# Performance work log

Measured on AMD Instinct MI355X. Metric: run time of the kernel, lower is better.

## Reference

```python
import jax, jax.numpy as jnp
import numpy as np

# Polynomial coefficients (len(thetas)=4 polys, k=3 -> 2 propagation hops each); K=1
THETAS = [[0.5, -0.4, 0.1], [0.25, 0.5, -0.25], [0.1, 0.3, 0.6], [0.05, -0.2, 0.8]]
K = 1
N_NODES = 100000
N_EDGES = 1600000
IN_FEATS = 32
OUT_FEATS = 64


def setup_inputs() -> dict:
    key = jax.random.key(0)
    ks = jax.random.split(key, 10)
    feat = jax.random.normal(ks[0], (N_NODES, IN_FEATS), dtype=jnp.float32)
    edge_src = jax.random.randint(ks[1], (N_EDGES,), 0, N_NODES)
    edge_dst = jax.random.randint(ks[2], (N_EDGES,), 0, N_NODES)
    labels = jax.random.randint(ks[3], (N_NODES,), 0, 2)
    s = 0.05
    W_lin = jax.random.normal(ks[4], (IN_FEATS * len(THETAS), OUT_FEATS), dtype=jnp.float32) * s
    b_lin = jax.random.normal(ks[5], (OUT_FEATS,), dtype=jnp.float32) * s
    W_lin1 = jax.random.normal(ks[6], (IN_FEATS * len(THETAS), OUT_FEATS), dtype=jnp.float32) * s
    b_lin1 = jax.random.normal(ks[7], (OUT_FEATS,), dtype=jnp.float32) * s
    W_transh = jax.random.normal(ks[8], (IN_FEATS, OUT_FEATS), dtype=jnp.float32) * s
    b_transh = jax.random.normal(ks[9], (OUT_FEATS,), dtype=jnp.float32) * s
    return {"feat": feat, "edge_src": edge_src, "edge_dst": edge_dst, "labels": labels,
            "W_lin": W_lin, "b_lin": b_lin, "W_lin1": W_lin1, "b_lin1": b_lin1,
            "W_transh": W_transh, "b_transh": b_transh}


def _poly_group(thetas, feat0, D_invsqrt, edge_src, edge_dst, mask, n_nodes):
    """Signed polynomial Laplacian propagation.
    Each hop: feat <- feat - scatter_sum_dst(mask * (feat*Dinv)[src]) * Dinv.
    feat carries over across thetas within a group (as in the original loop).
    """
    def prop(f):
        h = f * D_invsqrt                       # [N, F]
        m = h[edge_src]                         # gather [E, F]
        if mask is not None:
            m = m * mask[:, None]
        agg = jax.ops.segment_sum(m, edge_dst, num_segments=n_nodes)
        return f - agg * D_invsqrt

    hs = []
    f = feat0
    for th in thetas:
        h = th[0] * f
        for k in range(1, len(th)):
            f = prop(f)
            h = h + th[k] * f
        hs.append(h)
    return hs


def reference(feat, edge_src, edge_dst, labels, W_lin, b_lin, W_lin1, b_lin1, W_transh, b_transh):
    n_nodes = feat.shape[0]
    # edge sign from label agreement
    pos_mask = (labels[edge_src] == labels[edge_dst]).astype(feat.dtype)  # [E]
    neg_mask = 1.0 - pos_mask
    seg = lambda v: jax.ops.segment_sum(v, edge_dst, num_segments=n_nodes)
    deg = seg(jnp.ones_like(pos_mask))
    pos_deg = seg(pos_mask)
    neg_deg = seg(neg_mask)
    dinv = lambda d: jnp.power(jnp.clip(d, 1.0, None), -0.5)[:, None]
    D_o, D_p, D_n = dinv(deg), dinv(pos_deg), dinv(neg_deg)

    transh = feat @ W_transh + b_transh

    hs_o = _poly_group(THETAS, feat, D_o, edge_src, edge_dst, None, n_nodes)
    hs_p = _poly_group(THETAS[:K + 1], feat, D_p, edge_src, edge_dst, pos_mask, n_nodes)
    hs_n = _poly_group(THETAS[K + 1:], feat, D_n, edge_src, edge_dst, neg_mask, n_nodes)

    hs_o = jnp.concatenate(hs_o, axis=1)            # [N, F*len(thetas)]
    hs_pn = jnp.concatenate(hs_p + hs_n, axis=1)    # [N, F*len(thetas)]

    hs_o = jax.nn.leaky_relu(hs_o @ W_lin + b_lin, negative_slope=0.01)
    hs_pn = jax.nn.leaky_relu(hs_pn @ W_lin1 + b_lin1, negative_slope=0.01)
    return hs_o, hs_pn, transh
```

## Files before the change

### kernel.cpp

```cpp
#include <hip/hip_runtime.h>

#define N_NODES 100000
#define N_EDGES 1600000

typedef __attribute__((ext_vector_type(8))) unsigned short ushort8v;

#define OFF_G0    0UL
#define OFF_G1    19200000UL
#define OFF_HSO   38400000UL
#define OFF_HSPN  89600000UL
#define OFF_CSR   140800000UL
#define OFF_RP    147200000UL
#define OFF_CNT   147700000UL
#define OFF_CUR   148200000UL
#define OFF_D2O   149000000UL
#define OFF_D2P   149400000UL
#define OFF_D2N   149800000UL
#define OFF_RDO   150200000UL
#define OFF_RDP   150600000UL
#define OFF_RDN   151000000UL
#define OFF_DVO   151400000UL
#define OFF_DVP   151800000UL
#define OFF_DVN   152200000UL
#define OFF_PART  152600000UL

__device__ __forceinline__ float bf2f(unsigned short h) {
    union { unsigned u; float f; } c; c.u = ((unsigned)h) << 16; return c.f;
}
__device__ __forceinline__ unsigned short f2bf(float x) {
    union { float f; unsigned u; } c; c.f = x;
    unsigned r = (c.u + 0x7FFFu + ((c.u >> 16) & 1u)) >> 16;
    return (unsigned short)r;
}

__global__ __launch_bounds__(256) void k_mask_deg(
    const int* __restrict__ src, const int* __restrict__ dst,
    const int* __restrict__ labels, unsigned int* __restrict__ cnt) {
    int e = blockIdx.x * 256 + threadIdx.x;
    int s = src[e], d = dst[e];
    unsigned int p = (labels[s] == labels[d]) ? 1u : 0u;
    atomicAdd(&cnt[d], 0x10000u + p);
}

__global__ __launch_bounds__(256) void k_dinv(
    const unsigned int* __restrict__ cnt,
    float* __restrict__ d2o, float* __restrict__ d2p, float* __restrict__ d2n,
    float* __restrict__ rdo, float* __restrict__ rdp, float* __restrict__ rdn,
    float* __restrict__ dvo, float* __restrict__ dvp, float* __restrict__ dvn) {
    int v = blockIdx.x * 256 + threadIdx.x;
    if (v >= N_NODES) return;
    unsigned int c = cnt[v];
    int dg = (int)(c >> 16), pg = (int)(c & 0xFFFF), ng = dg - pg;
    float co = (float)max(dg, 1);
    float cp = (float)max(pg, 1);
    float cn = (float)max(ng, 1);
    d2o[v] = 1.f / co; rdo[v] = sqrtf(co); dvo[v] = rsqrtf(co);
    d2p[v] = 1.f / cp; rdp[v] = sqrtf(cp); dvp[v] = rsqrtf(cp);
    d2n[v] = 1.f / cn; rdn[v] = sqrtf(cn); dvn[v] = rsqrtf(cn);
}

__global__ __launch_bounds__(256) void k_scan_a(
    const unsigned int* __restrict__ cnt, int n, int* __restrict__ out,
    int* __restrict__ partial) {
    __shared__ int tmp[256];
    int g = blockIdx.x * 256 + threadIdx.x;
    int v = (g < n) ? (int)(cnt[g] >> 16) : 0;
    tmp[threadIdx.x] = v;
    __syncthreads();
    for (int off = 1; off < 256; off <<= 1) {
        int t = (threadIdx.x >= off) ? tmp[threadIdx.x - off] : 0;
        __syncthreads();
        tmp[threadIdx.x] += t;
        __syncthreads();
    }
    out[g] = tmp[threadIdx.x] - v;
    if (threadIdx.x == 255) partial[blockIdx.x] = tmp[255];
}

__global__ __launch_bounds__(512) void k_scan_b(int* __restrict__ partial, int nb) {
    __shared__ int tmp[512];
    int v = (threadIdx.x < nb) ? partial[threadIdx.x] : 0;
    tmp[threadIdx.x] = v;
    __syncthreads();
    for (int off = 1; off < 512; off <<= 1) {
        int t = (threadIdx.x >= off) ? tmp[threadIdx.x - off] : 0;
        __syncthreads();
        tmp[threadIdx.x] += t;
        __syncthreads();
    }
    if (threadIdx.x < nb) partial[threadIdx.x] = tmp[threadIdx.x] - v;
}

__global__ __launch_bounds__(256) void k_scan_c(
    int* __restrict__ out, const int* __restrict__ partial, int n,
    const unsigned int* __restrict__ cnt, unsigned long long* __restrict__ cur) {
    int g = blockIdx.x * 256 + threadIdx.x;
    int v = out[g] + partial[blockIdx.x];
    out[g] = v;
    if (g < n) {
        unsigned int curp = (unsigned int)v;
        unsigned int curn = (unsigned int)(v + (int)(cnt[g] & 0xFFFF));
        cur[g] = ((unsigned long long)curn << 32) | (unsigned long long)curp;
    }
}

__global__ __launch_bounds__(256) void k_fill(
    const int* __restrict__ src, const int* __restrict__ dst,
    const int* __restrict__ labels, unsigned long long* __restrict__ cur,
    unsigned int* __restrict__ csr) {
    int e = blockIdx.x * 256 + threadIdx.x;
    int s = src[e], d = dst[e];
    if (labels[s] == labels[d]) {
        unsigned long long old = atomicAdd(&cur[d], 1ULL);
        csr[(unsigned int)old] = (unsigned int)s;
    } else {
        unsigned long long old = atomicAdd(&cur[d], 1ULL << 32);
        csr[(unsigned int)(old >> 32)] = (unsigned int)s;
    }
}

__global__ __launch_bounds__(256) void k_init(
    const float* __restrict__ feat,
    const float* __restrict__ dvo, const float* __restrict__ dvp, const float* __restrict__ dvn,
    unsigned short* __restrict__ g0, float* __restrict__ hs_o, float* __restrict__ hs_pn) {
    int idx = blockIdx.x * 256 + threadIdx.x;
    int v = idx >> 5, c = idx & 31;
    float x = feat[idx];
    g0[v * 96 + c]      = f2bf(x * dvp[v]);
    g0[v * 96 + 32 + c] = f2bf(x * dvo[v]);
    g0[v * 96 + 64 + c] = f2bf(x * dvn[v]);
    hs_o[v * 128 + c]       = 0.5f * x;
    hs_pn[v * 128 + c]      = 0.5f * x;
    hs_pn[v * 128 + 64 + c] = 0.1f * x;
}

__global__ __launch_bounds__(256) void k_hop_fused(
    const int* __restrict__ rp, const unsigned int* __restrict__ cnt,
    const unsigned int* __restrict__ csr,
    const unsigned short* __restrict__ g_old, unsigned short* __restrict__ g_new,
    const float* __restrict__ d2o, const float* __restrict__ d2p, const float* __restrict__ d2n,
    const float* __restrict__ rdo, const float* __restrict__ rdp, const float* __restrict__ rdn,
    float* __restrict__ hs_o, float* __restrict__ hs_pn,
    int colAo, float cAo, int colBo, float cBo,
    int colAp, float cAp, int colBp, float cBp,
    int colAn, float cAn, int colBn, float cBn) {
    int v = (blockIdx.x * 256 + threadIdx.x) >> 6;
    int lane = threadIdx.x & 63;
    int slot = lane >> 3, fl = lane & 7;
    unsigned int c = cnt[v];
    int beg = rp[v];
    int mid = beg + (int)(c & 0xFFFF);
    int end = beg + (int)(c >> 16);
    const ushort8v* gp = reinterpret_cast<const ushort8v*>(g_old);
    float a1[8] = {0.f,0.f,0.f,0.f,0.f,0.f,0.f,0.f};
    float a2[8] = {0.f,0.f,0.f,0.f,0.f,0.f,0.f,0.f};
    for (int i = beg + slot; i < mid; i += 8) {
        int s = (int)csr[i];
        ushort8v h = gp[s * 12 + fl];
#pragma unroll
        for (int j = 0; j < 8; ++j) a1[j] += bf2f(h[j]);
    }
    for (int i = mid + slot; i < end; i += 8) {
        int s = (int)csr[i];
        ushort8v h = gp[s * 12 + 4 + fl];
#pragma unroll
        for (int j = 0; j < 8; ++j) a2[j] += bf2f(h[j]);
    }
#pragma unroll
    for (int m = 8; m < 64; m <<= 1)
#pragma unroll
        for (int j = 0; j < 8; ++j) {
            a1[j] += __shfl_xor(a1[j], m);
            a2[j] += __shfl_xor(a2[j], m);
        }
    float oextra[8];
    int srcl = (lane & 56) | ((fl + 4) & 7);
#pragma unroll
    for (int j = 0; j < 8; ++j) oextra[j] = __shfl(a2[j], srcl);

    if (lane < 4) {
        float dd = d2p[v], rr = rdp[v];
        ushort8v gh = gp[v * 12 + fl];
        ushort8v go; float fn[8];
#pragma unroll
        for (int j = 0; j < 8; ++j) {
            float gn = bf2f(gh[j]) - a1[j] * dd;
            go[j] = f2bf(gn); fn[j] = gn * rr;
        }
        reinterpret_cast<ushort8v*>(g_new)[v * 12 + fl] = go;
        float* hp = hs_pn + v * 128 + colAp + fl * 8;
#pragma unroll
        for (int j = 0; j < 8; ++j) hp[j] += cAp * fn[j];
        if (colBp >= 0) {
            float* bp = hs_pn + v * 128 + colBp + fl * 8;
#pragma unroll
            for (int j = 0; j < 8; ++j) bp[j] = cBp * fn[j];
        }
    } else if (lane < 8) {
        float dd = d2o[v], rr = rdo[v];
        ushort8v gh = gp[v * 12 + fl];
        ushort8v go; float fn[8];
#pragma unroll
        for (int j = 0; j < 8; ++j) {
            float gn = bf2f(gh[j]) - (a1[j] + oextra[j]) * dd;
            go[j] = f2bf(gn); fn[j] = gn * rr;
        }
        reinterpret_cast<ushort8v*>(g_new)[v * 12 + fl] = go;
        float* hp = hs_o + v * 128 + colAo + (fl - 4) * 8;
#pragma unroll
        for (int j = 0; j < 8; ++j) hp[j] += cAo * fn[j];
        if (colBo >= 0) {
            float* bp = hs_o + v * 128 + colBo + (fl - 4) * 8;
#pragma unroll
            for (int j = 0; j < 8; ++j) bp[j] = cBo * fn[j];
        }
    } else if (lane >= 12 && lane < 16) {
        float dd = d2n[v], rr = rdn[v];
        ushort8v gh = gp[v * 12 + fl + 4];
        ushort8v go; float fn[8];
#pragma unroll
        for (int j = 0; j < 8; ++j) {
            float gn = bf2f(gh[j]) - a2[j] * dd;
            go[j] = f2bf(gn); fn[j] = gn * rr;
        }
        reinterpret_cast<ushort8v*>(g_new)[v * 12 + fl + 4] = go;
        float* hp = hs_pn + v * 128 + colAn + (fl - 4) * 8;
#pragma unroll
        for (int j = 0; j < 8; ++j) hp[j] += cAn * fn[j];
        if (colBn >= 0) {
            float* bp = hs_pn + v * 128 + colBn + (fl - 4) * 8;
#pragma unroll
            for (int j = 0; j < 8; ++j) bp[j] = cBn * fn[j];
        }
    }
}

__global__ __launch_bounds__(256) void k_hop_o(
    const int* __restrict__ rp, const unsigned int* __restrict__ cnt,
    const unsigned int* __restrict__ csr,
    const unsigned short* __restrict__ g_old, unsigned short* __restrict__ g_new,
    const float* __restrict__ d2, const float* __restrict__ rd,
    float* __restrict__ hs, int colA, float cA, int colB, float cB) {
    int v = (blockIdx.x * 256 + threadIdx.x) >> 6;
    int lane = threadIdx.x & 63;
    int slot = lane >> 3, fl = lane & 7;
    int beg = rp[v];
    int end = beg + (int)(cnt[v] >> 16);
    const ushort4* gp = reinterpret_cast<const ushort4*>(g_old);
    float4 acc = make_float4(0.f, 0.f, 0.f, 0.f);
    for (int i = beg + slot; i < end; i += 8) {
        int s = (int)csr[i];
        ushort4 h = gp[s * 24 + 8 + fl];
        acc.x += bf2f(h.x); acc.y += bf2f(h.y);
        acc.z += bf2f(h.z); acc.w += bf2f(h.w);
    }
#pragma unroll
    for (int m = 8; m < 64; m <<= 1) {
        acc.x += __shfl_xor(acc.x, m);
        acc.y += __shfl_xor(acc.y, m);
        acc.z += __shfl_xor(acc.z, m);
        acc.w += __shfl_xor(acc.w, m);
    }
    if (slot == 0) {
        float dd = d2[v], rr = rd[v];
        ushort4 gh = gp[v * 24 + 8 + fl];
        float4 gn;
        gn.x = bf2f(gh.x) - acc.x * dd; gn.y = bf2f(gh.y) - acc.y * dd;
        gn.z = bf2f(gh.z) - acc.z * dd; gn.w = bf2f(gh.w) - acc.w * dd;
        ushort4 go;
        go.x = f2bf(gn.x); go.y = f2bf(gn.y); go.z = f2bf(gn.z); go.w = f2bf(gn.w);
        reinterpret_cast<ushort4*>(g_new)[v * 24 + 8 + fl] = go;
        float4 fn;
        fn.x = gn.x * rr; fn.y = gn.y * rr; fn.z = gn.z * rr; fn.w = gn.w * rr;
        float4* hp = reinterpret_cast<float4*>(hs + v * 128 + colA) + fl;
        float4 h = *hp;
        h.x += cA * fn.x; h.y += cA * fn.y; h.z += cA * fn.z; h.w += cA * fn.w;
        *hp = h;
        if (colB >= 0) {
            reinterpret_cast<float4*>(hs + v * 128 + colB)[fl] =
                make_float4(cB * fn.x, cB * fn.y, cB * fn.z, cB * fn.w);
        }
    }
}

template <int KDIM, bool RELU>
__global__ __launch_bounds__(256) void k_gemm(
    const float* __restrict__ X, const float* __restrict__ W,
    const float* __restrict__ bias, float* __restrict__ out, int nrows) {
    constexpr int SXP = KDIM + 4;
    __shared__ float sW[KDIM * 64];
    __shared__ float sX[64 * SXP];
    int tid = threadIdx.x;
    int rowbase = blockIdx.x * 64;

    for (int i = tid; i < KDIM * 16; i += 256)
        reinterpret_cast<float4*>(sW)[i] = reinterpret_cast<const float4*>(W)[i];

    constexpr int QF4 = KDIM / 4;
    constexpr int RPP = 256 / QF4;
    int q = tid & (QF4 - 1);
    int rloc = tid / QF4;
#pragma unroll
    for (int pass = 0; pass < 64 / RPP; ++pass) {
        int r = rloc + pass * RPP;
        int rg = rowbase + r;
        float4 v = make_float4(0.f, 0.f, 0.f, 0.f);
        if (rg < nrows) v = reinterpret_cast<const float4*>(X + (size_t)rg * KDIM)[q];
        float* dst = sX + r * SXP + q * 4;
        dst[0] = v.x; dst[1] = v.y; dst[2] = v.z; dst[3] = v.w;
    }
    __syncthreads();

    int c0 = (tid & 15) * 4;
    int r0 = (tid >> 4) * 4;
    float4 bv = reinterpret_cast<const float4*>(bias)[tid & 15];
    float4 acc0 = bv, acc1 = bv, acc2 = bv, acc3 = bv;

#pragma unroll 4
    for (int k4 = 0; k4 < KDIM / 4; ++k4) {
        int k = k4 * 4;
        float4 x0 = *reinterpret_cast<const float4*>(sX + (r0 + 0) * SXP + k);
        float4 x1 = *reinterpret_cast<const float4*>(sX + (r0 + 1) * SXP + k);
        float4 x2 = *reinterpret_cast<const float4*>(sX + (r0 + 2) * SXP + k);
        float4 x3 = *reinterpret_cast<const float4*>(sX + (r0 + 3) * SXP + k);
        float4 w0 = *reinterpret_cast<const float4*>(sW + (k + 0) * 64 + c0);
        float4 w1 = *reinterpret_cast<const float4*>(sW + (k + 1) * 64 + c0);
        float4 w2 = *reinterpret_cast<const float4*>(sW + (k + 2) * 64 + c0);
        float4 w3 = *reinterpret_cast<const float4*>(sW + (k + 3) * 64 + c0);
#define FMA4(A, xs, wv) \
        A.x = fmaf(xs, wv.x, A.x); A.y = fmaf(xs, wv.y, A.y); \
        A.z = fmaf(xs, wv.z, A.z); A.w = fmaf(xs, wv.w, A.w);
        FMA4(acc0, x0.x, w0) FMA4(acc0, x0.y, w1) FMA4(acc0, x0.z, w2) FMA4(acc0, x0.w, w3)
        FMA4(acc1, x1.x, w0) FMA4(acc1, x1.y, w1) FMA4(acc1, x1.z, w2) FMA4(acc1, x1.w, w3)
        FMA4(acc2, x2.x, w0) FMA4(acc2, x2.y, w1) FMA4(acc2, x2.z, w2) FMA4(acc2, x2.w, w3)
        FMA4(acc3, x3.x, w0) FMA4(acc3, x3.y, w1) FMA4(acc3, x3.z, w2) FMA4(acc3, x3.w, w3)
#undef FMA4
    }

#define EPI(A, i) { \
        int rg = rowbase + r0 + i; \
        if (rg < nrows) { \
            if (RELU) { \
                A.x = A.x > 0.f ? A.x : 0.01f * A.x; \
                A.y = A.y > 0.f ? A.y : 0.01f * A.y; \
                A.z = A.z > 0.f ? A.z : 0.01f * A.z; \
                A.w = A.w > 0.f ? A.w : 0.01f * A.w; \
            } \
            *reinterpret_cast<float4*>(out + (size_t)rg * 64 + c0) = A; \
        } }
    EPI(acc0, 0) EPI(acc1, 1) EPI(acc2, 2) EPI(acc3, 3)
#undef EPI
}

extern "C" void kernel_launch(void* const* d_in, const int* in_sizes, int n_in,
                              void* d_out, int out_size, void* d_ws, size_t ws_size,
                              hipStream_t stream) {
    const float* feat   = (const float*)d_in[0];
    const int*   esrc   = (const int*)d_in[1];
    const int*   edst   = (const int*)d_in[2];
    const int*   labels = (const int*)d_in[3];
    const float* W_lin  = (const float*)d_in[4];
    const float* b_lin  = (const float*)d_in[5];
    const float* W_lin1 = (const float*)d_in[6];
    const float* b_lin1 = (const float*)d_in[7];
    const float* W_th   = (const float*)d_in[8];
    const float* b_th   = (const float*)d_in[9];

    char* ws = (char*)d_ws;
    unsigned short* g0 = (unsigned short*)(ws + OFF_G0);
    unsigned short* g1 = (unsigned short*)(ws + OFF_G1);
    float* hs_o  = (float*)(ws + OFF_HSO);
    float* hs_pn = (float*)(ws + OFF_HSPN);
    unsigned int* csr = (unsigned int*)(ws + OFF_CSR);
    int* rp     = (int*)(ws + OFF_RP);
    unsigned int* cnt = (unsigned int*)(ws + OFF_CNT);
    unsigned long long* cur = (unsigned long long*)(ws + OFF_CUR);
    float* d2o  = (float*)(ws + OFF_D2O);
    float* d2p  = (float*)(ws + OFF_D2P);
    float* d2n  = (float*)(ws + OFF_D2N);
    float* rdo  = (float*)(ws + OFF_RDO);
    float* rdp  = (float*)(ws + OFF_RDP);
    float* rdn  = (float*)(ws + OFF_RDN);
    float* dvo  = (float*)(ws + OFF_DVO);
    float* dvp  = (float*)(ws + OFF_DVP);
    float* dvn  = (float*)(ws + OFF_DVN);
    int* part   = (int*)(ws + OFF_PART);

    float* out0 = (float*)d_out;
    float* out1 = out0 + (size_t)N_NODES * 64;
    float* out2 = out1 + (size_t)N_NODES * 64;

    const float TH[4][3] = {{0.5f, -0.4f, 0.1f},
                            {0.25f, 0.5f, -0.25f},
                            {0.1f, 0.3f, 0.6f},
                            {0.05f, -0.2f, 0.8f}};

    const int EB = N_EDGES / 256;
    const int NB = (N_NODES + 255) / 256;
    const int SB = (N_NODES + 255) / 256 + 1;
    const int HB = N_NODES / 4;
    const int GB = (N_NODES + 63) / 64;

    hipMemsetAsync(cnt, 0, N_NODES * sizeof(int), stream);
    k_mask_deg<<<EB, 256, 0, stream>>>(esrc, edst, labels, cnt);
    k_dinv<<<NB, 256, 0, stream>>>(cnt, d2o, d2p, d2n, rdo, rdp, rdn, dvo, dvp, dvn);

    k_scan_a<<<SB, 256, 0, stream>>>(cnt, N_NODES, rp, part);
    k_scan_b<<<1, 512, 0, stream>>>(part, SB);
    k_scan_c<<<SB, 256, 0, stream>>>(rp, part, N_NODES, cnt, cur);
    k_fill<<<EB, 256, 0, stream>>>(esrc, edst, labels, cur, csr);

    k_init<<<N_NODES * 32 / 256, 256, 0, stream>>>(feat, dvo, dvp, dvn, g0, hs_o, hs_pn);

    unsigned short* ga = g0; unsigned short* gb = g1;
    for (int hop = 0; hop < 4; ++hop) {
        int poly = hop >> 1, kk = (hop & 1) + 1;
        int colAo = poly * 32;       float cAo = TH[poly][kk];
        int colAp = poly * 32;       float cAp = TH[poly][kk];
        int colAn = 64 + poly * 32;  float cAn = TH[poly + 2][kk];
        int colBo = -1, colBp = -1, colBn = -1;
        float cBo = 0.f, cBp = 0.f, cBn = 0.f;
        if (kk == 2) {
            colBo = (poly + 1) * 32; cBo = TH[poly + 1][0];
            if (poly == 0) { colBp = 32; cBp = TH[1][0]; colBn = 96; cBn = TH[3][0]; }
        }
        k_hop_fused<<<HB, 256, 0, stream>>>(rp, cnt, csr, ga, gb,
                                            d2o, d2p, d2n, rdo, rdp, rdn, hs_o, hs_pn,
                                            colAo, cAo, colBo, cBo,
                                            colAp, cAp, colBp, cBp,
                                            colAn, cAn, colBn, cBn);
        unsigned short* t = ga; ga = gb; gb = t;
    }
    k_gemm<128, true><<<GB, 256, 0, stream>>>(hs_pn, W_lin1, b_lin1, out1, N_NODES);

    for (int hop = 4; hop < 8; ++hop) {
        int poly = hop >> 1, kk = (hop & 1) + 1;
        int colA = poly * 32;
        float cA = TH[poly][kk];
        int colB = -1; float cB = 0.f;
        if (kk == 2 && poly < 3) { colB = (poly + 1) * 32; cB = TH[poly + 1][0]; }
        k_hop_o<<<HB, 256, 0, stream>>>(rp, cnt, csr, ga, gb, d2o, rdo, hs_o, colA, cA, colB, cB);
        unsigned short* t = ga; ga = gb; gb = t;
    }
    k_gemm<128, true><<<GB, 256, 0, stream>>>(hs_o, W_lin, b_lin, out0, N_NODES);

    k_gemm<32, false><<<GB, 256, 0, stream>>>(feat, W_th, b_th, out2, N_NODES);
}
```

Measured before the change: 803.3 us.

## Fold polynomial coefficients into weights and keep all hop states instead of hs accumulators

The per-hop read-modify-write of the fp32 hs_o/hs_pn accumulators is removed. Each hop's bf16 propagated state is now kept in its own buffer. The theta coefficients are folded into combined weight matrices by small precompute kernels, and a new double-buffered GEMM streams the stored hop slices, rescaling each by sqrt(deg) while loading it. This removes the scattered fp32 accumulator traffic from the hop kernels. In exchange the GEMM has to read 9–10 bf16 slices and the workspace grows.

```diff
diff --git a/kernel.cpp b/kernel.cpp
--- a/kernel.cpp
+++ b/kernel.cpp
@@ -5,24 +5,31 @@
 
 typedef __attribute__((ext_vector_type(8))) unsigned short ushort8v;
 
-#define OFF_G0    0UL
-#define OFF_G1    19200000UL
-#define OFF_HSO   38400000UL
-#define OFF_HSPN  89600000UL
-#define OFF_CSR   140800000UL
-#define OFF_RP    147200000UL
-#define OFF_CNT   147700000UL
-#define OFF_CUR   148200000UL
-#define OFF_D2O   149000000UL
-#define OFF_D2P   149400000UL
-#define OFF_D2N   149800000UL
-#define OFF_RDO   150200000UL
-#define OFF_RDP   150600000UL
-#define OFF_RDN   151000000UL
-#define OFF_DVO   151400000UL
-#define OFF_DVP   151800000UL
-#define OFF_DVN   152200000UL
-#define OFF_PART  152600000UL
+#define OFF_F0    0UL
+#define OFF_F1    19200000UL
+#define OFF_F2    38400000UL
+#define OFF_F3    57600000UL
+#define OFF_F4    76800000UL
+#define OFF_O5    96000000UL
+#define OFF_O6    102400000UL
+#define OFF_O7    108800000UL
+#define OFF_O8    115200000UL
+#define OFF_CSR   121600000UL
+#define OFF_RP    128000000UL
+#define OFF_CNT   128500000UL
+#define OFF_CUR   129000000UL
+#define OFF_D2O   129800000UL
+#define OFF_D2P   130200000UL
+#define OFF_D2N   130600000UL
+#define OFF_RDO   131000000UL
+#define OFF_RDP   131400000UL
+#define OFF_RDN   131800000UL
+#define OFF_DVO   132200000UL
+#define OFF_DVP   132600000UL
+#define OFF_DVN   133000000UL
+#define OFF_WCO   133400000UL
+#define OFF_WCPN  133480000UL
+#define OFF_PART  133570000UL
 
 __device__ __forceinline__ float bf2f(unsigned short h) {
     union { unsigned u; float f; } c; c.u = ((unsigned)h) << 16; return c.f;
@@ -32,6 +39,10 @@
     unsigned r = (c.u + 0x7FFFu + ((c.u >> 16) & 1u)) >> 16;
     return (unsigned short)r;
 }
+
+__device__ __constant__ float c_TH[4][3] = {
+    {0.5f, -0.4f, 0.1f}, {0.25f, 0.5f, -0.25f},
+    {0.1f, 0.3f, 0.6f}, {0.05f, -0.2f, 0.8f}};
 
 __global__ __launch_bounds__(256) void k_mask_deg(
     const int* __restrict__ src, const int* __restrict__ dst,
@@ -59,6 +70,41 @@
     d2n[v] = 1.f / cn; rdn[v] = sqrtf(cn); dvn[v] = rsqrtf(cn);
 }
 
+__global__ __launch_bounds__(256) void k_wc_o(const float* __restrict__ W, float* __restrict__ Wc) {
+    int idx = blockIdx.x * 256 + threadIdx.x;
+    if (idx >= 9 * 2048) return;
+    int k = idx >> 11, rem = idx & 2047, r = rem >> 6, c = rem & 63;
+    float v = 0.f;
+#pragma unroll
+    for (int j = 0; j < 4; ++j) {
+        int m = k - 2 * j;
+        if (m >= 0 && m <= 2) v += c_TH[j][m] * W[(32 * j + r) * 64 + c];
+    }
+    Wc[idx] = v;
+}
+
+__global__ __launch_bounds__(256) void k_wc_pn(const float* __restrict__ W1, float* __restrict__ Wc) {
+    int idx = blockIdx.x * 256 + threadIdx.x;
+    if (idx >= 10 * 2048) return;
+    int k5 = idx >> 11, rem = idx & 2047, r = rem >> 6, c = rem & 63;
+    float v = 0.f;
+    if (k5 < 5) {
+#pragma unroll
+        for (int j = 0; j < 2; ++j) {
+            int m = k5 - 2 * j;
+            if (m >= 0 && m <= 2) v += c_TH[j][m] * W1[(32 * j + r) * 64 + c];
+        }
+    } else {
+        int k = k5 - 5;
+#pragma unroll
+        for (int j = 0; j < 2; ++j) {
+            int m = k - 2 * j;
+            if (m >= 0 && m <= 2) v += c_TH[2 + j][m] * W1[(32 * (j + 2) + r) * 64 + c];
+        }
+    }
+    Wc[idx] = v;
+}
+
 __global__ __launch_bounds__(256) void k_scan_a(
     const unsigned int* __restrict__ cnt, int n, int* __restrict__ out,
     int* __restrict__ partial) {
@@ -122,28 +168,20 @@
 __global__ __launch_bounds__(256) void k_init(
     const float* __restrict__ feat,
     const float* __restrict__ dvo, const float* __restrict__ dvp, const float* __restrict__ dvn,
-    unsigned short* __restrict__ g0, float* __restrict__ hs_o, float* __restrict__ hs_pn) {
+    unsigned short* __restrict__ g0) {
     int idx = blockIdx.x * 256 + threadIdx.x;
     int v = idx >> 5, c = idx & 31;
     float x = feat[idx];
     g0[v * 96 + c]      = f2bf(x * dvp[v]);
     g0[v * 96 + 32 + c] = f2bf(x * dvo[v]);
     g0[v * 96 + 64 + c] = f2bf(x * dvn[v]);
-    hs_o[v * 128 + c]       = 0.5f * x;
-    hs_pn[v * 128 + c]      = 0.5f * x;
-    hs_pn[v * 128 + 64 + c] = 0.1f * x;
 }
 
 __global__ __launch_bounds__(256) void k_hop_fused(
     const int* __restrict__ rp, const unsigned int* __restrict__ cnt,
     const unsigned int* __restrict__ csr,
     const unsigned short* __restrict__ g_old, unsigned short* __restrict__ g_new,
-    const float* __restrict__ d2o, const float* __restrict__ d2p, const float* __restrict__ d2n,
-    const float* __restrict__ rdo, const float* __restrict__ rdp, const float* __restrict__ rdn,
-    float* __restrict__ hs_o, float* __restrict__ hs_pn,
-    int colAo, float cAo, int colBo, float cBo,
-    int colAp, float cAp, int colBp, float cBp,
-    int colAn, float cAn, int colBn, float cBn) {
+    const float* __restrict__ d2o, const float* __restrict__ d2p, const float* __restrict__ d2n) {
     int v = (blockIdx.x * 256 + threadIdx.x) >> 6;
     int lane = threadIdx.x & 63;
     int slot = lane >> 3, fl = lane & 7;
@@ -179,68 +217,34 @@
     for (int j = 0; j < 8; ++j) oextra[j] = __shfl(a2[j], srcl);
 
     if (lane < 4) {
-        float dd = d2p[v], rr = rdp[v];
+        float dd = d2p[v];
         ushort8v gh = gp[v * 12 + fl];
-        ushort8v go; float fn[8];
-#pragma unroll
-        for (int j = 0; j < 8; ++j) {
-            float gn = bf2f(gh[j]) - a1[j] * dd;
-            go[j] = f2bf(gn); fn[j] = gn * rr;
-        }
+        ushort8v go;
+#pragma unroll
+        for (int j = 0; j < 8; ++j) go[j] = f2bf(bf2f(gh[j]) - a1[j] * dd);
         reinterpret_cast<ushort8v*>(g_new)[v * 12 + fl] = go;
-        float* hp = hs_pn + v * 128 + colAp + fl * 8;
-#pragma unroll
-        for (int j = 0; j < 8; ++j) hp[j] += cAp * fn[j];
-        if (colBp >= 0) {
-            float* bp = hs_pn + v * 128 + colBp + fl * 8;
-#pragma unroll
-            for (int j = 0; j < 8; ++j) bp[j] = cBp * fn[j];
-        }
     } else if (lane < 8) {
-        float dd = d2o[v], rr = rdo[v];
+        float dd = d2o[v];
         ushort8v gh = gp[v * 12 + fl];
-        ushort8v go; float fn[8];
-#pragma unroll
-        for (int j = 0; j < 8; ++j) {
-            float gn = bf2f(gh[j]) - (a1[j] + oextra[j]) * dd;
-            go[j] = f2bf(gn); fn[j] = gn * rr;
-        }
+        ushort8v go;
+#pragma unroll
+        for (int j = 0; j < 8; ++j) go[j] = f2bf(bf2f(gh[j]) - (a1[j] + oextra[j]) * dd);
         reinterpret_cast<ushort8v*>(g_new)[v * 12 + fl] = go;
-        float* hp = hs_o + v * 128 + colAo + (fl - 4) * 8;
-#pragma unroll
-        for (int j = 0; j < 8; ++j) hp[j] += cAo * fn[j];
-        if (colBo >= 0) {
-            float* bp = hs_o + v * 128 + colBo + (fl - 4) * 8;
-#pragma unroll
-            for (int j = 0; j < 8; ++j) bp[j] = cBo * fn[j];
-        }
     } else if (lane >= 12 && lane < 16) {
-        float dd = d2n[v], rr = rdn[v];
+        float dd = d2n[v];
         ushort8v gh = gp[v * 12 + fl + 4];
-        ushort8v go; float fn[8];
-#pragma unroll
-        for (int j = 0; j < 8; ++j) {
-            float gn = bf2f(gh[j]) - a2[j] * dd;
-            go[j] = f2bf(gn); fn[j] = gn * rr;
-        }
+        ushort8v go;
+#pragma unroll
+        for (int j = 0; j < 8; ++j) go[j] = f2bf(bf2f(gh[j]) - a2[j] * dd);
         reinterpret_cast<ushort8v*>(g_new)[v * 12 + fl + 4] = go;
-        float* hp = hs_pn + v * 128 + colAn + (fl - 4) * 8;
-#pragma unroll
-        for (int j = 0; j < 8; ++j) hp[j] += cAn * fn[j];
-        if (colBn >= 0) {
-            float* bp = hs_pn + v * 128 + colBn + (fl - 4) * 8;
-#pragma unroll
-            for (int j = 0; j < 8; ++j) bp[j] = cBn * fn[j];
-        }
     }
 }
 
 __global__ __launch_bounds__(256) void k_hop_o(
     const int* __restrict__ rp, const unsigned int* __restrict__ cnt,
     const unsigned int* __restrict__ csr,
-    const unsigned short* __restrict__ g_old, unsigned short* __restrict__ g_new,
-    const float* __restrict__ d2, const float* __restrict__ rd,
-    float* __restrict__ hs, int colA, float cA, int colB, float cB) {
+    const unsigned short* __restrict__ g_old, int stride_u4,
+    unsigned short* __restrict__ g_new, const float* __restrict__ d2) {
     int v = (blockIdx.x * 256 + threadIdx.x) >> 6;
     int lane = threadIdx.x & 63;
     int slot = lane >> 3, fl = lane & 7;
@@ -250,7 +254,7 @@
     float4 acc = make_float4(0.f, 0.f, 0.f, 0.f);
     for (int i = beg + slot; i < end; i += 8) {
         int s = (int)csr[i];
-        ushort4 h = gp[s * 24 + 8 + fl];
+        ushort4 h = gp[s * stride_u4 + fl];
         acc.x += bf2f(h.x); acc.y += bf2f(h.y);
         acc.z += bf2f(h.z); acc.w += bf2f(h.w);
     }
@@ -262,25 +266,92 @@
         acc.w += __shfl_xor(acc.w, m);
     }
     if (slot == 0) {
-        float dd = d2[v], rr = rd[v];
-        ushort4 gh = gp[v * 24 + 8 + fl];
-        float4 gn;
-        gn.x = bf2f(gh.x) - acc.x * dd; gn.y = bf2f(gh.y) - acc.y * dd;
-        gn.z = bf2f(gh.z) - acc.z * dd; gn.w = bf2f(gh.w) - acc.w * dd;
+        float dd = d2[v];
+        ushort4 gh = gp[v * stride_u4 + fl];
         ushort4 go;
-        go.x = f2bf(gn.x); go.y = f2bf(gn.y); go.z = f2bf(gn.z); go.w = f2bf(gn.w);
-        reinterpret_cast<ushort4*>(g_new)[v * 24 + 8 + fl] = go;
-        float4 fn;
-        fn.x = gn.x * rr; fn.y = gn.y * rr; fn.z = gn.z * rr; fn.w = gn.w * rr;
-        float4* hp = reinterpret_cast<float4*>(hs + v * 128 + colA) + fl;
-        float4 h = *hp;
-        h.x += cA * fn.x; h.y += cA * fn.y; h.z += cA * fn.z; h.w += cA * fn.w;
-        *hp = h;
-        if (colB >= 0) {
-            reinterpret_cast<float4*>(hs + v * 128 + colB)[fl] =
-                make_float4(cB * fn.x, cB * fn.y, cB * fn.z, cB * fn.w);
+        go.x = f2bf(bf2f(gh.x) - acc.x * dd);
+        go.y = f2bf(bf2f(gh.y) - acc.y * dd);
+        go.z = f2bf(bf2f(gh.z) - acc.z * dd);
+        go.w = f2bf(bf2f(gh.w) - acc.w * dd);
+        reinterpret_cast<ushort4*>(g_new)[v * 8 + fl] = go;
+    }
+}
+
+struct SliceArgs { const unsigned short* ptr[10]; int stride[10]; };
+
+template <int NS>
+__global__ __launch_bounds__(256) void k_gemm_fold(
+    SliceArgs sl, const float* __restrict__ scA, const float* __restrict__ scB, int nA,
+    const float* __restrict__ Wc, const float* __restrict__ bias,
+    float* __restrict__ out, int nrows) {
+    __shared__ float sX[2][64 * 36];
+    __shared__ float sW[2][2048];
+    int tid = threadIdx.x;
+    int rowbase = blockIdx.x * 64;
+    int u = tid & 3, rr = tid >> 2;
+    int rgs = rowbase + rr;
+
+#define STAGE(k, b) { \
+        float sc = 0.f; ushort8v h = (ushort8v)0; \
+        if (rgs < nrows) { \
+            sc = ((k) < nA) ? scA[rgs] : scB[rgs]; \
+            h = reinterpret_cast<const ushort8v*>(sl.ptr[k] + (size_t)rgs * sl.stride[k])[u]; \
+        } \
+        float* dx = &sX[b][rr * 36 + u * 8]; \
+        _Pragma("unroll") \
+        for (int j = 0; j < 8; ++j) dx[j] = bf2f(h[j]) * sc; \
+        const float4* wsrc = reinterpret_cast<const float4*>(Wc + (k) * 2048); \
+        float4* wdst = reinterpret_cast<float4*>(sW[b]); \
+        for (int i = tid; i < 512; i += 256) wdst[i] = wsrc[i]; \
+    }
+
+    int c0 = (tid & 15) * 4;
+    int r0 = (tid >> 4) * 4;
+    float4 acc0 = reinterpret_cast<const float4*>(bias)[tid & 15];
+    float4 acc1 = acc0, acc2 = acc0, acc3 = acc0;
+
+    STAGE(0, 0);
+    int buf = 0;
+    for (int k = 0; k < NS; ++k) {
+        __syncthreads();
+        if (k + 1 < NS) STAGE(k + 1, buf ^ 1);
+        const float* xb = sX[buf];
+        const float* wb = sW[buf];
+#pragma unroll
+        for (int k4 = 0; k4 < 8; ++k4) {
+            int kk = k4 * 4;
+            float4 x0 = *reinterpret_cast<const float4*>(xb + (r0 + 0) * 36 + kk);
+            float4 x1 = *reinterpret_cast<const float4*>(xb + (r0 + 1) * 36 + kk);
+            float4 x2 = *reinterpret_cast<const float4*>(xb + (r0 + 2) * 36 + kk);
+            float4 x3 = *reinterpret_cast<const float4*>(xb + (r0 + 3) * 36 + kk);
+            float4 w0 = *reinterpret_cast<const float4*>(wb + (kk + 0) * 64 + c0);
+            float4 w1 = *reinterpret_cast<const float4*>(wb + (kk + 1) * 64 + c0);
+            float4 w2 = *reinterpret_cast<const float4*>(wb + (kk + 2) * 64 + c0);
+            float4 w3 = *reinterpret_cast<const float4*>(wb + (kk + 3) * 64 + c0);
+#define FMA4(A, xs, wv) \
+            A.x = fmaf(xs, wv.x, A.x); A.y = fmaf(xs, wv.y, A.y); \
+            A.z = fmaf(xs, wv.z, A.z); A.w = fmaf(xs, wv.w, A.w);
+            FMA4(acc0, x0.x, w0) FMA4(acc0, x0.y, w1) FMA4(acc0, x0.z, w2) FMA4(acc0, x0.w, w3)
+            FMA4(acc1, x1.x, w0) FMA4(acc1, x1.y, w1) FMA4(acc1, x1.z, w2) FMA4(acc1, x1.w, w3)
+            FMA4(acc2, x2.x, w0) FMA4(acc2, x2.y, w1) FMA4(acc2, x2.z, w2) FMA4(acc2, x2.w, w3)
+            FMA4(acc3, x3.x, w0) FMA4(acc3, x3.y, w1) FMA4(acc3, x3.z, w2) FMA4(acc3, x3.w, w3)
+#undef FMA4
         }
-    }
+        buf ^= 1;
+    }
+#undef STAGE
+
+#define EPI(A, i) { \
+        int rg = rowbase + r0 + i; \
+        if (rg < nrows) { \
+            A.x = A.x > 0.f ? A.x : 0.01f * A.x; \
+            A.y = A.y > 0.f ? A.y : 0.01f * A.y; \
+            A.z = A.z > 0.f ? A.z : 0.01f * A.z; \
+            A.w = A.w > 0.f ? A.w : 0.01f * A.w; \
+            *reinterpret_cast<float4*>(out + (size_t)rg * 64 + c0) = A; \
+        } }
+    EPI(acc0, 0) EPI(acc1, 1) EPI(acc2, 2) EPI(acc3, 3)
+#undef EPI
 }
 
 template <int KDIM, bool RELU>
@@ -292,10 +363,8 @@
     __shared__ float sX[64 * SXP];
     int tid = threadIdx.x;
     int rowbase = blockIdx.x * 64;
-
     for (int i = tid; i < KDIM * 16; i += 256)
         reinterpret_cast<float4*>(sW)[i] = reinterpret_cast<const float4*>(W)[i];
-
     constexpr int QF4 = KDIM / 4;
     constexpr int RPP = 256 / QF4;
     int q = tid & (QF4 - 1);
@@ -310,12 +379,10 @@
         dst[0] = v.x; dst[1] = v.y; dst[2] = v.z; dst[3] = v.w;
     }
     __syncthreads();
-
     int c0 = (tid & 15) * 4;
     int r0 = (tid >> 4) * 4;
     float4 bv = reinterpret_cast<const float4*>(bias)[tid & 15];
     float4 acc0 = bv, acc1 = bv, acc2 = bv, acc3 = bv;
-
 #pragma unroll 4
     for (int k4 = 0; k4 < KDIM / 4; ++k4) {
         int k = k4 * 4;
@@ -336,7 +403,6 @@
         FMA4(acc3, x3.x, w0) FMA4(acc3, x3.y, w1) FMA4(acc3, x3.z, w2) FMA4(acc3, x3.w, w3)
 #undef FMA4
     }
-
 #define EPI(A, i) { \
         int rg = rowbase + r0 + i; \
         if (rg < nrows) { \
@@ -367,10 +433,13 @@
     const float* b_th   = (const float*)d_in[9];
 
     char* ws = (char*)d_ws;
-    unsigned short* g0 = (unsigned short*)(ws + OFF_G0);
-    unsigned short* g1 = (unsigned short*)(ws + OFF_G1);
-    float* hs_o  = (float*)(ws + OFF_HSO);
-    float* hs_pn = (float*)(ws + OFF_HSPN);
+    unsigned short* F[5] = {
+        (unsigned short*)(ws + OFF_F0), (unsigned short*)(ws + OFF_F1),
+        (unsigned short*)(ws + OFF_F2), (unsigned short*)(ws + OFF_F3),
+        (unsigned short*)(ws + OFF_F4)};
+    unsigned short* O[4] = {
+        (unsigned short*)(ws + OFF_O5), (unsigned short*)(ws + OFF_O6),
+        (unsigned short*)(ws + OFF_O7), (unsigned short*)(ws + OFF_O8)};
     unsigned int* csr = (unsigned int*)(ws + OFF_CSR);
     int* rp     = (int*)(ws + OFF_RP);
     unsigned int* cnt = (unsigned int*)(ws + OFF_CNT);
@@ -384,16 +453,13 @@
     float* dvo  = (float*)(ws + OFF_DVO);
     float* dvp  = (float*)(ws + OFF_DVP);
     float* dvn  = (float*)(ws + OFF_DVN);
+    float* wco  = (float*)(ws + OFF_WCO);
+    float* wcpn = (float*)(ws + OFF_WCPN);
     int* part   = (int*)(ws + OFF_PART);
 
     float* out0 = (float*)d_out;
     float* out1 = out0 + (size_t)N_NODES * 64;
     float* out2 = out1 + (size_t)N_NODES * 64;
-
-    const float TH[4][3] = {{0.5f, -0.4f, 0.1f},
-                            {0.25f, 0.5f, -0.25f},
-                            {0.1f, 0.3f, 0.6f},
-                            {0.05f, -0.2f, 0.8f}};
 
     const int EB = N_EDGES / 256;
     const int NB = (N_NODES + 255) / 256;
@@ -410,39 +476,32 @@
     k_scan_c<<<SB, 256, 0, stream>>>(rp, part, N_NODES, cnt, cur);
     k_fill<<<EB, 256, 0, stream>>>(esrc, edst, labels, cur, csr);
 
-    k_init<<<N_NODES * 32 / 256, 256, 0, stream>>>(feat, dvo, dvp, dvn, g0, hs_o, hs_pn);
-
-    unsigned short* ga = g0; unsigned short* gb = g1;
-    for (int hop = 0; hop < 4; ++hop) {
-        int poly = hop >> 1, kk = (hop & 1) + 1;
-        int colAo = poly * 32;       float cAo = TH[poly][kk];
-        int colAp = poly * 32;       float cAp = TH[poly][kk];
-        int colAn = 64 + poly * 32;  float cAn = TH[poly + 2][kk];
-        int colBo = -1, colBp = -1, colBn = -1;
-        float cBo = 0.f, cBp = 0.f, cBn = 0.f;
-        if (kk == 2) {
-            colBo = (poly + 1) * 32; cBo = TH[poly + 1][0];
-            if (poly == 0) { colBp = 32; cBp = TH[1][0]; colBn = 96; cBn = TH[3][0]; }
-        }
-        k_hop_fused<<<HB, 256, 0, stream>>>(rp, cnt, csr, ga, gb,
-                                            d2o, d2p, d2n, rdo, rdp, rdn, hs_o, hs_pn,
-                                            colAo, cAo, colBo, cBo,
-                                            colAp, cAp, colBp, cBp,
-                                            colAn, cAn, colBn, cBn);
-        unsigned short* t = ga; ga = gb; gb = t;
-    }
-    k_gemm<128, true><<<GB, 256, 0, stream>>>(hs_pn, W_lin1, b_lin1, out1, N_NODES);
-
-    for (int hop = 4; hop < 8; ++hop) {
-        int poly = hop >> 1, kk = (hop & 1) + 1;
-        int colA = poly * 32;
-        float cA = TH[poly][kk];
-        int colB = -1; float cB = 0.f;
-        if (kk == 2 && poly < 3) { colB = (poly + 1) * 32; cB = TH[poly + 1][0]; }
-        k_hop_o<<<HB, 256, 0, stream>>>(rp, cnt, csr, ga, gb, d2o, rdo, hs_o, colA, cA, colB, cB);
-        unsigned short* t = ga; ga = gb; gb = t;
-    }
-    k_gemm<128, true><<<GB, 256, 0, stream>>>(hs_o, W_lin, b_lin, out0, N_NODES);
+    k_wc_o<<<72, 256, 0, stream>>>(W_lin, wco);
+    k_wc_pn<<<80, 256, 0, stream>>>(W_lin1, wcpn);
+
+    k_init<<<N_NODES * 32 / 256, 256, 0, stream>>>(feat, dvo, dvp, dvn, F[0]);
+
+    for (int k = 1; k <= 4; ++k)
+        k_hop_fused<<<HB, 256, 0, stream>>>(rp, cnt, csr, F[k - 1], F[k], d2o, d2p, d2n);
+
+    {
+        SliceArgs sl;
+        for (int k = 0; k < 5; ++k) { sl.ptr[k] = F[k];      sl.stride[k] = 96; }
+        for (int k = 0; k < 5; ++k) { sl.ptr[5 + k] = F[k] + 64; sl.stride[5 + k] = 96; }
+        k_gemm_fold<10><<<GB, 256, 0, stream>>>(sl, rdp, rdn, 5, wcpn, b_lin1, out1, N_NODES);
+    }
+
+    k_hop_o<<<HB, 256, 0, stream>>>(rp, cnt, csr, F[4] + 32, 24, O[0], d2o);
+    for (int k = 1; k < 4; ++k)
+        k_hop_o<<<HB, 256, 0, stream>>>(rp, cnt, csr, O[k - 1], 8, O[k], d2o);
+
+    {
+        SliceArgs sl;
+        for (int k = 0; k < 5; ++k) { sl.ptr[k] = F[k] + 32; sl.stride[k] = 96; }
+        for (int k = 0; k < 4; ++k) { sl.ptr[5 + k] = O[k];  sl.stride[5 + k] = 32; }
+        sl.ptr[9] = O[0]; sl.stride[9] = 32;
+        k_gemm_fold<9><<<GB, 256, 0, stream>>>(sl, rdo, rdo, 9, wco, b_lin, out0, N_NODES);
+    }
 
     k_gemm<32, false><<<GB, 256, 0, stream>>>(feat, W_th, b_th, out2, N_NODES);
 }
```

Result: faster. 778.4 us (-3.1%).
